# Kernel tuning notes

Hardware: AMD Instinct MI355X
Metric: run time of the kernel (lower is better)

The kernel has to match this reference:

```python
import jax, jax.numpy as jnp
import numpy as np

N, E, IN, HID, OUT = 50000, 800000, 128, 96, 2


def setup_inputs() -> dict:
    key = jax.random.key(0)
    ks = jax.random.split(key, 10)
    x = jax.random.normal(ks[0], (N, IN), jnp.float32)
    edge_index = jax.random.randint(ks[1], (2, E), 0, N, dtype=jnp.int64)
    # PQVA mask: per-node, first output channel is a "known" quantity (masked out),
    # second is the prediction target -> ~mask selects exactly N elements.
    m = np.zeros((N, OUT), dtype=bool)
    m[:, 0] = True
    PQVA_mask = jnp.asarray(m)
    scaler_mean = 0.1 * jax.random.normal(ks[2], (IN,), jnp.float32)
    scaler_std = 0.5 + jax.random.uniform(ks[3], (IN,), jnp.float32)  # in [0.5, 1.5)
    W1 = jax.random.normal(ks[4], (IN, HID), jnp.float32) / np.sqrt(IN)
    W2 = jax.random.normal(ks[5], (HID, HID), jnp.float32) / np.sqrt(HID)
    W3 = jax.random.normal(ks[6], (HID, HID), jnp.float32) / np.sqrt(HID)
    Wout = jax.random.normal(ks[7], (HID, OUT), jnp.float32) / np.sqrt(HID)
    b1 = jnp.zeros((HID,), jnp.float32)
    b2 = jnp.zeros((HID,), jnp.float32)
    b3 = jnp.zeros((HID,), jnp.float32)
    bout = jnp.zeros((OUT,), jnp.float32)
    return {"x": x, "edge_index": edge_index, "PQVA_mask": PQVA_mask,
            "scaler_mean": scaler_mean, "scaler_std": scaler_std,
            "W1": W1, "b1": b1, "W2": W2, "b2": b2, "W3": W3, "b3": b3,
            "Wout": Wout, "bout": bout}


def reference(x, edge_index, PQVA_mask, scaler_mean, scaler_std,
              W1, b1, W2, b2, W3, b3, Wout, bout):
    n = x.shape[0]
    loop = jnp.arange(n, dtype=edge_index.dtype)
    src = jnp.concatenate([edge_index[0], loop])  # add self-loops (GCNConv default)
    dst = jnp.concatenate([edge_index[1], loop])
    deg = jax.ops.segment_sum(jnp.ones_like(dst, x.dtype), dst, num_segments=n)
    dinv = jax.lax.rsqrt(deg)  # deg >= 1 thanks to self-loops
    norm = (dinv[src] * dinv[dst])[:, None]  # [E+N, 1]

    def prop(h):  # D^-1/2 (A+I) D^-1/2 @ h  via gather-scale-scatter
        return jax.ops.segment_sum(h[src] * norm, dst, num_segments=n)

    h = (x - scaler_mean) / scaler_std          # standard scaler
    h = jax.nn.relu(prop(h @ W1) + b1)          # GCNConv 1 + ReLU
    h = jax.nn.relu(prop(h @ W2) + b2)          # GCNConv 2 + ReLU
    h = prop(h @ W3) + b3                       # GCNConv 3 (last, no act)
    out = h @ Wout + bout                       # final Linear -> [N, OUT]
    # masked reshape: ~mask has exactly one True per node -> [N]
    return out.reshape(-1)[~PQVA_mask.reshape(-1)]
```

## Files before the change

kernel.cpp:

```cpp
#include <hip/hip_runtime.h>
#include <hip/hip_fp16.h>

#define IN_F 128
#define HID_F 96
#define PB 512
#define STRIDE 6144
#define MAXB 8192

typedef _Float16 f16x8 __attribute__((ext_vector_type(8)));
typedef float f32x4 __attribute__((ext_vector_type(4)));

__device__ __forceinline__ void swizzle_one(const float* W, __half* Wsw, int idx) {
    int j  = idx & 7;
    int ln = (idx >> 3) & 63;
    int ct = idx >> 9;
    int t = ct % 6, c = ct / 6;
    int k   = c * 32 + (ln >> 4) * 8 + j;
    int col = t * 16 + (ln & 15);
    Wsw[idx] = (__half)W[k * 96 + col];
}

__global__ __launch_bounds__(256) void part_prep_kernel(
        const int* __restrict__ srcv, const int* __restrict__ dstv,
        int* __restrict__ bcur, int* __restrict__ ebuf, int E,
        const float* __restrict__ stdv, float* __restrict__ rstd,
        const float* __restrict__ W3, const float* __restrict__ Wout,
        const float* __restrict__ b3, const float* __restrict__ bout,
        float* __restrict__ wv, float* __restrict__ cconst,
        const float* __restrict__ W1, __half* __restrict__ Wsw1, int SW1,
        const float* __restrict__ W2, __half* __restrict__ Wsw2, int SW2) {
    int b = blockIdx.x, t = threadIdx.x;
    if (b >= PB) {
        int pb = b - PB;
        if (pb == 0) {
            if (t < IN_F) rstd[t] = 1.0f / stdv[t];
            if (t < HID_F) {
                float s = 0.f;
                for (int j = 0; j < HID_F; ++j) s += W3[t * HID_F + j] * Wout[j * 2 + 1];
                wv[t] = s;
            }
            if (t == 0) {
                float s = 0.f;
                for (int j = 0; j < HID_F; ++j) s += b3[j] * Wout[j * 2 + 1];
                cconst[0] = s + bout[1];
            }
        } else if (pb <= 48) {
            int idx = (pb - 1) * 256 + t;
            if (idx < SW1) swizzle_one(W1, Wsw1, idx);
        } else {
            int idx = (pb - 49) * 256 + t;
            if (idx < SW2) swizzle_one(W2, Wsw2, idx);
        }
        return;
    }
    __shared__ int h[256];
    __shared__ int cur[256];
    int chunk = (E + PB - 1) / PB;
    int s = b * chunk;
    int eend = min(s + chunk, E);
    h[t] = 0;
    __syncthreads();
    for (int e = s + t; e < eend; e += 256) atomicAdd(&h[dstv[e] >> 8], 1);
    __syncthreads();
    if (h[t]) cur[t] = t * STRIDE + atomicAdd(&bcur[t], h[t]);
    __syncthreads();
    for (int e = s + t; e < eend; e += 256) {
        int sv = srcv[e], d = dstv[e];
        int p = atomicAdd(&cur[d >> 8], 1);
        ebuf[p] = (sv << 8) | (d & 255);
    }
}


template<int MODE, int K, int SC>
__device__ __forceinline__ void gemm_body(
        int bid, int tid,
        const void* __restrict__ Ain, const __half* __restrict__ Wsw,
        const float* __restrict__ mean, const float* __restrict__ rstd,
        const float* __restrict__ dinv, __half* __restrict__ C, int n) {
    constexpr int NCH = K / 32;
    int lane = tid & 63;
    int wv_  = tid >> 6;
    int m = lane & 15, q = lane >> 4;
    int node0 = bid * 64 + wv_ * 16;
    int g = node0 + m;
    int gc = g < n ? g : n - 1;

    f32x4 acc[6];
#pragma unroll
    for (int t = 0; t < 6; ++t) acc[t] = (f32x4){0.f, 0.f, 0.f, 0.f};

#pragma unroll
    for (int c = 0; c < NCH; ++c) {
        f16x8 a;
        if (MODE == 0) {
            const float* ap = (const float*)Ain + (long)gc * K + c * 32 + q * 8;
            float4 v0 = *(const float4*)ap;
            float4 v1 = *(const float4*)(ap + 4);
            float4 m0 = *(const float4*)(mean + c * 32 + q * 8);
            float4 m1 = *(const float4*)(mean + c * 32 + q * 8 + 4);
            float4 r0 = *(const float4*)(rstd + c * 32 + q * 8);
            float4 r1 = *(const float4*)(rstd + c * 32 + q * 8 + 4);
            a[0] = (_Float16)((v0.x - m0.x) * r0.x);
            a[1] = (_Float16)((v0.y - m0.y) * r0.y);
            a[2] = (_Float16)((v0.z - m0.z) * r0.z);
            a[3] = (_Float16)((v0.w - m0.w) * r0.w);
            a[4] = (_Float16)((v1.x - m1.x) * r1.x);
            a[5] = (_Float16)((v1.y - m1.y) * r1.y);
            a[6] = (_Float16)((v1.z - m1.z) * r1.z);
            a[7] = (_Float16)((v1.w - m1.w) * r1.w);
        } else {
            a = *(const f16x8*)((const __half*)Ain + (long)gc * K + c * 32 + q * 8);
        }
#pragma unroll
        for (int t = 0; t < 6; ++t) {
            f16x8 b = *(const f16x8*)(Wsw + (size_t)(((c * 6) + t) * 64 + lane) * 8);
            acc[t] = __builtin_amdgcn_mfma_f32_16x16x32_f16(a, b, acc[t], 0, 0, 0);
        }
    }
    float dv[4];
#pragma unroll
    for (int r = 0; r < 4; ++r) {
        int gr = node0 + q * 4 + r;
        dv[r] = SC ? ((gr < n) ? dinv[gr] : 0.f) : 1.f;
    }
#pragma unroll
    for (int t = 0; t < 6; ++t)
#pragma unroll
        for (int r = 0; r < 4; ++r) {
            int gr = node0 + q * 4 + r;
            float o = SC ? acc[t][r] * dv[r] : acc[t][r];
            if (gr < n) C[(long)gr * 96 + t * 16 + m] = (__half)o;
        }
}

template<int MODE, int K, int SC>
__global__ __launch_bounds__(256) void gemm_mfma_kernel(
        const void* __restrict__ Ain, const __half* __restrict__ Wsw,
        const float* __restrict__ mean, const float* __restrict__ rstd,
        const float* __restrict__ dinv, __half* __restrict__ C, int n) {
    gemm_body<MODE, K, SC>(blockIdx.x, threadIdx.x, Ain, Wsw, mean, rstd, dinv, C, n);
}


__global__ __launch_bounds__(256) void csr_gemm1_kernel(
        const int* __restrict__ ebuf, const int* __restrict__ bcur,
        int* __restrict__ rowdeg, float* __restrict__ dinv,
        int* __restrict__ cols, int n, int nb,
        const float* __restrict__ x, const __half* __restrict__ Wsw1,
        const float* __restrict__ mean, const float* __restrict__ rstd,
        __half* __restrict__ C) {
    __shared__ int dg[256];
    __shared__ int tmp[256];
    __shared__ int cur[256];
    __shared__ int colst[MAXB];
    int t = threadIdx.x;
    if (blockIdx.x >= nb) {
        gemm_body<0, IN_F, 0>(blockIdx.x - nb, t, x, Wsw1, mean, rstd, nullptr, C, n);
        return;
    }
    int k = blockIdx.x;
    int seg = k * STRIDE;
    int cnt = min(bcur[k], STRIDE);
    dg[t] = 0;
    __syncthreads();
    for (int i = t; i < cnt; i += 256) atomicAdd(&dg[ebuf[seg + i] & 255], 1);
    __syncthreads();
    int v = dg[t];
    tmp[t] = v;
    __syncthreads();
#pragma unroll
    for (int off = 1; off < 256; off <<= 1) {
        int u = (t >= off) ? tmp[t - off] : 0;
        __syncthreads();
        tmp[t] += u;
        __syncthreads();
    }
    int excl = tmp[t] - v;
    int node = (k << 8) + t;
    if (node < n) {
        rowdeg[node] = ((seg + excl) << 9) | v;
        dinv[node] = rsqrtf((float)v + 1.0f);
    }
    cur[t] = excl;
    __syncthreads();
    for (int i = t; i < cnt; i += 256) {
        int p = ebuf[seg + i];
        int lp = atomicAdd(&cur[p & 255], 1);
        colst[lp] = ((unsigned)p) >> 8;
    }
    __syncthreads();
    for (int i = t; i < cnt; i += 256) cols[seg + i] = colst[i];
}


template<int DOT, int SCALE>
__global__ __launch_bounds__(256) void prop4_kernel(
        const __half* __restrict__ hin, const int* __restrict__ rowdeg,
        const int* __restrict__ cols,
        const float* __restrict__ dinv, const float* __restrict__ bias,
        const float* __restrict__ wvv, __half* __restrict__ hout,
        float* __restrict__ zs, int n) {
    int wid  = (blockIdx.x * blockDim.x + threadIdx.x) >> 6;
    int lane = threadIdx.x & 63;
    int g = lane >> 4;
    int l = lane & 15;
    int node = wid * 4 + g;
    bool nvalid = node < n;
    int nodec = nvalid ? node : n - 1;
    int rd = rowdeg[nodec];
    int e0 = ((unsigned)rd) >> 9;
    int deg = rd & 511;
    float di = dinv[nodec];
    const f16x8* hp = (const f16x8*)hin;
    int lc = l < 12 ? l : 0;

    f16x8 vself = hp[(long)nodec * 12 + lc];
    float sself = SCALE ? di : 1.f;
    float acc[8];
#pragma unroll
    for (int j = 0; j < 8; ++j) acc[j] = sself * (float)vself[j];

    for (int eb = 0; eb < deg; eb += 16) {
        int rem = deg - eb;
        if (rem > 16) rem = 16;
        int idx = eb + l;
        int colv = __builtin_nontemporal_load(&cols[e0 + (idx < deg ? idx : 0)]);
        float dvl = SCALE ? dinv[colv] : 1.f;
        for (int k0 = 0; k0 < rem; k0 += 8) {
            int c[8];
            float s[8];
#pragma unroll
            for (int kk = 0; kk < 8; ++kk) {
                int p = k0 + kk;
                int srcl = (g << 4) + p;
                int cc = __shfl(colv, srcl, 64);
                float dd = __shfl(dvl, srcl, 64);
                bool is = p < rem;
                c[kk] = is ? cc : nodec;
                s[kk] = is ? (SCALE ? dd : 1.f) : 0.f;
            }
            f16x8 v[8];
#pragma unroll
            for (int kk = 0; kk < 8; ++kk) v[kk] = hp[(long)c[kk] * 12 + lc];
#pragma unroll
            for (int kk = 0; kk < 8; ++kk)
#pragma unroll
                for (int j = 0; j < 8; ++j)
                    acc[j] = fmaf((float)v[kk][j], s[kk], acc[j]);
        }
    }

    if (DOT == 0) {
        if (nvalid && l < 12) {
            float4 b0 = *(const float4*)(bias + l * 8);
            float4 b1 = *(const float4*)(bias + l * 8 + 4);
            f16x8 o;
            o[0] = (_Float16)fmaxf(di * acc[0] + b0.x, 0.f);
            o[1] = (_Float16)fmaxf(di * acc[1] + b0.y, 0.f);
            o[2] = (_Float16)fmaxf(di * acc[2] + b0.z, 0.f);
            o[3] = (_Float16)fmaxf(di * acc[3] + b0.w, 0.f);
            o[4] = (_Float16)fmaxf(di * acc[4] + b1.x, 0.f);
            o[5] = (_Float16)fmaxf(di * acc[5] + b1.y, 0.f);
            o[6] = (_Float16)fmaxf(di * acc[6] + b1.z, 0.f);
            o[7] = (_Float16)fmaxf(di * acc[7] + b1.w, 0.f);
            __builtin_nontemporal_store(o, (f16x8*)(hout + (long)node * 96 + l * 8));
        }
    } else {
        float v = 0.f;
        if (l < 12) {
            float4 b0 = *(const float4*)(bias + l * 8);
            float4 b1 = *(const float4*)(bias + l * 8 + 4);
            float4 w0 = *(const float4*)(wvv + l * 8);
            float4 w1 = *(const float4*)(wvv + l * 8 + 4);
            v  = fmaxf(di * acc[0] + b0.x, 0.f) * w0.x;
            v += fmaxf(di * acc[1] + b0.y, 0.f) * w0.y;
            v += fmaxf(di * acc[2] + b0.z, 0.f) * w0.z;
            v += fmaxf(di * acc[3] + b0.w, 0.f) * w0.w;
            v += fmaxf(di * acc[4] + b1.x, 0.f) * w1.x;
            v += fmaxf(di * acc[5] + b1.y, 0.f) * w1.y;
            v += fmaxf(di * acc[6] + b1.z, 0.f) * w1.z;
            v += fmaxf(di * acc[7] + b1.w, 0.f) * w1.w;
        }
        v += __shfl_xor(v, 1, 64);
        v += __shfl_xor(v, 2, 64);
        v += __shfl_xor(v, 4, 64);
        v += __shfl_xor(v, 8, 64);
        if (nvalid && l == 0) __builtin_nontemporal_store(di * v, &zs[node]);
    }
}


__global__ __launch_bounds__(256) void prop_scalar_kernel(
        const float* __restrict__ zs, const int* __restrict__ rowdeg,
        const int* __restrict__ cols,
        const float* __restrict__ dinv, const float* __restrict__ cconst,
        float* __restrict__ out, int n) {
    int i = blockIdx.x * blockDim.x + threadIdx.x;
    if (i >= n) return;
    int rd = rowdeg[i];
    int e0 = ((unsigned)rd) >> 9;
    int e1 = e0 + (rd & 511);
    float s = 0.f;
    int e = e0;
    for (; e + 8 <= e1; e += 8) {
        int c[8];
#pragma unroll
        for (int k = 0; k < 8; ++k) c[k] = __builtin_nontemporal_load(&cols[e + k]);
        float z[8];
#pragma unroll
        for (int k = 0; k < 8; ++k) z[k] = zs[c[k]];
#pragma unroll
        for (int k = 0; k < 8; ++k) s += z[k];
    }
    for (; e < e1; ++e) s += zs[__builtin_nontemporal_load(&cols[e])];
    out[i] = dinv[i] * (s + zs[i]) + cconst[0];
}


extern "C" void kernel_launch(void* const* d_in, const int* in_sizes, int n_in,
                              void* d_out, int out_size, void* d_ws, size_t ws_size,
                              hipStream_t stream) {
    const float* x    = (const float*)d_in[0];
    const int*   eidx = (const int*)d_in[1];
    const float* mean = (const float*)d_in[3];
    const float* stdv = (const float*)d_in[4];
    const float* W1   = (const float*)d_in[5];
    const float* b1   = (const float*)d_in[6];
    const float* W2   = (const float*)d_in[7];
    const float* b2   = (const float*)d_in[8];
    const float* W3   = (const float*)d_in[9];
    const float* b3   = (const float*)d_in[10];
    const float* Wout = (const float*)d_in[11];
    const float* bout = (const float*)d_in[12];
    float* out = (float*)d_out;

    const int n = in_sizes[0] / IN_F;
    const int E = in_sizes[1] / 2;
    const int* srcv = eidx;
    const int* dstv = eidx + E;
    const int NB = (n + 255) >> 8;

    char* ws = (char*)d_ws;
    size_t off = 0;
    auto alloc = [&](size_t bytes) -> void* {
        void* p = ws + off;
        off = (off + bytes + 255) & ~(size_t)255;
        return p;
    };
    const int SW1 = 4 * 6 * 64 * 8;
    const int SW2 = 3 * 6 * 64 * 8;
    int*    rowdeg = (int*)alloc((size_t)n * 4);
    float*  dinv   = (float*)alloc((size_t)n * 4);
    int*    cols   = (int*)alloc((size_t)256 * STRIDE * 4);
    int*    ebuf   = (int*)alloc((size_t)256 * STRIDE * 4);
    int*    bcur   = (int*)alloc(256 * 4);
    float*  rstd   = (float*)alloc(IN_F * 4);
    float*  wv     = (float*)alloc(HID_F * 4);
    float*  cconst = (float*)alloc(4);
    float*  zbuf   = (float*)alloc((size_t)n * 4);
    __half* Wsw1   = (__half*)alloc((size_t)SW1 * 2);
    __half* Wsw2   = (__half*)alloc((size_t)SW2 * 2);
    __half* bufA   = (__half*)alloc((size_t)n * HID_F * 2);
    __half* bufB   = (__half*)alloc((size_t)n * HID_F * 2);

    hipMemsetAsync(bcur, 0, 256 * 4, stream);

    part_prep_kernel<<<PB + 85, 256, 0, stream>>>(
        srcv, dstv, bcur, ebuf, E,
        stdv, rstd, W3, Wout, b3, bout, wv, cconst,
        W1, Wsw1, SW1, W2, Wsw2, SW2);

    int gemm_grid = (n + 63) / 64;
    int wpg = (n + 3) / 4;
    int prop_grid = (int)(((long)wpg * 64 + 255) / 256);

    csr_gemm1_kernel<<<NB + gemm_grid, 256, 0, stream>>>(
        ebuf, bcur, rowdeg, dinv, cols, n, NB, x, Wsw1, mean, rstd, bufA);

    prop4_kernel<0, 1><<<prop_grid, 256, 0, stream>>>(bufA, rowdeg, cols, dinv, b1,
                                                      nullptr, bufB, nullptr, n);
    gemm_mfma_kernel<1, HID_F, 1><<<gemm_grid, 256, 0, stream>>>(
        bufB, Wsw2, nullptr, nullptr, dinv, bufA, n);
    prop4_kernel<1, 0><<<prop_grid, 256, 0, stream>>>(bufA, rowdeg, cols, dinv, b2,
                                                      wv, nullptr, zbuf, n);
    prop_scalar_kernel<<<(n + 255) / 256, 256, 0, stream>>>(zbuf, rowdeg, cols, dinv,
                                                            cconst, out, n);
}
```

Baseline: 195.3 us.

## Fuse all GCN stages into one cooperative persistent kernel with grid syncs

Replaces the chain of six kernel launches with a single cooperative persistent kernel whose blocks grid-stride over each stage (partition, CSR build plus first GEMM, two propagations, second GEMM, scalar propagation), separated by grid.sync(). The goal is to remove launch gaps and tail idle time between dependent stages. The cost is grid-wide barriers and a grid capped at 2048 blocks with occupancy hint 4, which may reduce latency hiding in the gather-heavy propagation phases. The shared colst array shrinks from 8192 to STRIDE entries. If the cooperative launch fails, the original separate kernels run instead.

```diff
diff --git a/kernel.cpp b/kernel.cpp
--- a/kernel.cpp
+++ b/kernel.cpp
@@ -1,11 +1,16 @@
 #include <hip/hip_runtime.h>
 #include <hip/hip_fp16.h>
+#include <hip/hip_cooperative_groups.h>
+
+namespace cg = cooperative_groups;
 
 #define IN_F 128
 #define HID_F 96
 #define PB 512
 #define STRIDE 6144
-#define MAXB 8192
+#define SW1C (4 * 6 * 64 * 8)
+#define SW2C (3 * 6 * 64 * 8)
+#define ONE_PASS (1 << 22)
 
 typedef _Float16 f16x8 __attribute__((ext_vector_type(8)));
 typedef float f32x4 __attribute__((ext_vector_type(4)));
@@ -20,57 +25,100 @@
     Wsw[idx] = (__half)W[k * 96 + col];
 }
 
-__global__ __launch_bounds__(256) void part_prep_kernel(
+__device__ __forceinline__ void p0_body(int b0, int bstep, int t,
         const int* __restrict__ srcv, const int* __restrict__ dstv,
         int* __restrict__ bcur, int* __restrict__ ebuf, int E,
         const float* __restrict__ stdv, float* __restrict__ rstd,
         const float* __restrict__ W3, const float* __restrict__ Wout,
         const float* __restrict__ b3, const float* __restrict__ bout,
         float* __restrict__ wv, float* __restrict__ cconst,
-        const float* __restrict__ W1, __half* __restrict__ Wsw1, int SW1,
-        const float* __restrict__ W2, __half* __restrict__ Wsw2, int SW2) {
-    int b = blockIdx.x, t = threadIdx.x;
-    if (b >= PB) {
-        int pb = b - PB;
-        if (pb == 0) {
-            if (t < IN_F) rstd[t] = 1.0f / stdv[t];
-            if (t < HID_F) {
-                float s = 0.f;
-                for (int j = 0; j < HID_F; ++j) s += W3[t * HID_F + j] * Wout[j * 2 + 1];
-                wv[t] = s;
-            }
-            if (t == 0) {
-                float s = 0.f;
-                for (int j = 0; j < HID_F; ++j) s += b3[j] * Wout[j * 2 + 1];
-                cconst[0] = s + bout[1];
-            }
-        } else if (pb <= 48) {
-            int idx = (pb - 1) * 256 + t;
-            if (idx < SW1) swizzle_one(W1, Wsw1, idx);
-        } else {
-            int idx = (pb - 49) * 256 + t;
-            if (idx < SW2) swizzle_one(W2, Wsw2, idx);
-        }
-        return;
-    }
+        const float* __restrict__ W1, __half* __restrict__ Wsw1,
+        const float* __restrict__ W2, __half* __restrict__ Wsw2) {
     __shared__ int h[256];
     __shared__ int cur[256];
-    int chunk = (E + PB - 1) / PB;
-    int s = b * chunk;
-    int eend = min(s + chunk, E);
-    h[t] = 0;
-    __syncthreads();
-    for (int e = s + t; e < eend; e += 256) atomicAdd(&h[dstv[e] >> 8], 1);
-    __syncthreads();
-    if (h[t]) cur[t] = t * STRIDE + atomicAdd(&bcur[t], h[t]);
-    __syncthreads();
-    for (int e = s + t; e < eend; e += 256) {
-        int sv = srcv[e], d = dstv[e];
-        int p = atomicAdd(&cur[d >> 8], 1);
-        ebuf[p] = (sv << 8) | (d & 255);
-    }
-}
-
+    for (int b = b0; b < PB + 85; b += bstep) {
+        if (b >= PB) {
+            int pb = b - PB;
+            if (pb == 0) {
+                if (t < IN_F) rstd[t] = 1.0f / stdv[t];
+                if (t < HID_F) {
+                    float s = 0.f;
+                    for (int j = 0; j < HID_F; ++j) s += W3[t * HID_F + j] * Wout[j * 2 + 1];
+                    wv[t] = s;
+                }
+                if (t == 0) {
+                    float s = 0.f;
+                    for (int j = 0; j < HID_F; ++j) s += b3[j] * Wout[j * 2 + 1];
+                    cconst[0] = s + bout[1];
+                }
+            } else if (pb <= 48) {
+                int idx = (pb - 1) * 256 + t;
+                if (idx < SW1C) swizzle_one(W1, Wsw1, idx);
+            } else {
+                int idx = (pb - 49) * 256 + t;
+                if (idx < SW2C) swizzle_one(W2, Wsw2, idx);
+            }
+            continue;
+        }
+        int chunk = (E + PB - 1) / PB;
+        int s = b * chunk;
+        int eend = min(s + chunk, E);
+        h[t] = 0;
+        __syncthreads();
+        for (int e = s + t; e < eend; e += 256) atomicAdd(&h[dstv[e] >> 8], 1);
+        __syncthreads();
+        if (h[t]) cur[t] = t * STRIDE + atomicAdd(&bcur[t], h[t]);
+        __syncthreads();
+        for (int e = s + t; e < eend; e += 256) {
+            int sv = srcv[e], d = dstv[e];
+            int p = atomicAdd(&cur[d >> 8], 1);
+            ebuf[p] = (sv << 8) | (d & 255);
+        }
+        __syncthreads();
+    }
+}
+
+__device__ __forceinline__ void csr_body(int k, int t,
+        const int* __restrict__ ebuf, const int* __restrict__ bcur,
+        int* __restrict__ rowdeg, float* __restrict__ dinv,
+        int* __restrict__ cols, int n) {
+    __shared__ int dg[256];
+    __shared__ int tmp[256];
+    __shared__ int cur[256];
+    __shared__ int colst[STRIDE];
+    int seg = k * STRIDE;
+    int cnt = min(bcur[k], STRIDE);
+    dg[t] = 0;
+    __syncthreads();
+    for (int i = t; i < cnt; i += 256) atomicAdd(&dg[ebuf[seg + i] & 255], 1);
+    __syncthreads();
+    int v = dg[t];
+    tmp[t] = v;
+    __syncthreads();
+#pragma unroll
+    for (int off = 1; off < 256; off <<= 1) {
+        int u = (t >= off) ? tmp[t - off] : 0;
+        __syncthreads();
+        tmp[t] += u;
+        __syncthreads();
+    }
+    int excl = tmp[t] - v;
+    int node = (k << 8) + t;
+    if (node < n) {
+        rowdeg[node] = ((seg + excl) << 9) | v;
+        dinv[node] = rsqrtf((float)v + 1.0f);
+    }
+    cur[t] = excl;
+    __syncthreads();
+    for (int i = t; i < cnt; i += 256) {
+        int p = ebuf[seg + i];
+        int lp = atomicAdd(&cur[p & 255], 1);
+        colst[lp] = ((unsigned)p) >> 8;
+    }
+    __syncthreads();
+    for (int i = t; i < cnt; i += 256) cols[seg + i] = colst[i];
+    __syncthreads();
+}
 
 template<int MODE, int K, int SC>
 __device__ __forceinline__ void gemm_body(
@@ -134,189 +182,198 @@
         }
 }
 
-template<int MODE, int K, int SC>
-__global__ __launch_bounds__(256) void gemm_mfma_kernel(
-        const void* __restrict__ Ain, const __half* __restrict__ Wsw,
-        const float* __restrict__ mean, const float* __restrict__ rstd,
-        const float* __restrict__ dinv, __half* __restrict__ C, int n) {
-    gemm_body<MODE, K, SC>(blockIdx.x, threadIdx.x, Ain, Wsw, mean, rstd, dinv, C, n);
-}
-
-
-__global__ __launch_bounds__(256) void csr_gemm1_kernel(
-        const int* __restrict__ ebuf, const int* __restrict__ bcur,
-        int* __restrict__ rowdeg, float* __restrict__ dinv,
-        int* __restrict__ cols, int n, int nb,
-        const float* __restrict__ x, const __half* __restrict__ Wsw1,
-        const float* __restrict__ mean, const float* __restrict__ rstd,
-        __half* __restrict__ C) {
-    __shared__ int dg[256];
-    __shared__ int tmp[256];
-    __shared__ int cur[256];
-    __shared__ int colst[MAXB];
-    int t = threadIdx.x;
-    if (blockIdx.x >= nb) {
-        gemm_body<0, IN_F, 0>(blockIdx.x - nb, t, x, Wsw1, mean, rstd, nullptr, C, n);
-        return;
-    }
-    int k = blockIdx.x;
-    int seg = k * STRIDE;
-    int cnt = min(bcur[k], STRIDE);
-    dg[t] = 0;
-    __syncthreads();
-    for (int i = t; i < cnt; i += 256) atomicAdd(&dg[ebuf[seg + i] & 255], 1);
-    __syncthreads();
-    int v = dg[t];
-    tmp[t] = v;
-    __syncthreads();
-#pragma unroll
-    for (int off = 1; off < 256; off <<= 1) {
-        int u = (t >= off) ? tmp[t - off] : 0;
-        __syncthreads();
-        tmp[t] += u;
-        __syncthreads();
-    }
-    int excl = tmp[t] - v;
-    int node = (k << 8) + t;
-    if (node < n) {
-        rowdeg[node] = ((seg + excl) << 9) | v;
-        dinv[node] = rsqrtf((float)v + 1.0f);
-    }
-    cur[t] = excl;
-    __syncthreads();
-    for (int i = t; i < cnt; i += 256) {
-        int p = ebuf[seg + i];
-        int lp = atomicAdd(&cur[p & 255], 1);
-        colst[lp] = ((unsigned)p) >> 8;
-    }
-    __syncthreads();
-    for (int i = t; i < cnt; i += 256) cols[seg + i] = colst[i];
-}
-
-
 template<int DOT, int SCALE>
-__global__ __launch_bounds__(256) void prop4_kernel(
+__device__ __forceinline__ void prop_body(int b0, int bstep, int t,
         const __half* __restrict__ hin, const int* __restrict__ rowdeg,
         const int* __restrict__ cols,
         const float* __restrict__ dinv, const float* __restrict__ bias,
         const float* __restrict__ wvv, __half* __restrict__ hout,
         float* __restrict__ zs, int n) {
-    int wid  = (blockIdx.x * blockDim.x + threadIdx.x) >> 6;
-    int lane = threadIdx.x & 63;
+    int wv_  = t >> 6;
+    int lane = t & 63;
     int g = lane >> 4;
     int l = lane & 15;
-    int node = wid * 4 + g;
-    bool nvalid = node < n;
-    int nodec = nvalid ? node : n - 1;
-    int rd = rowdeg[nodec];
-    int e0 = ((unsigned)rd) >> 9;
-    int deg = rd & 511;
-    float di = dinv[nodec];
+    int lc = l < 12 ? l : 0;
     const f16x8* hp = (const f16x8*)hin;
-    int lc = l < 12 ? l : 0;
-
-    f16x8 vself = hp[(long)nodec * 12 + lc];
-    float sself = SCALE ? di : 1.f;
-    float acc[8];
-#pragma unroll
-    for (int j = 0; j < 8; ++j) acc[j] = sself * (float)vself[j];
-
-    for (int eb = 0; eb < deg; eb += 16) {
-        int rem = deg - eb;
-        if (rem > 16) rem = 16;
-        int idx = eb + l;
-        int colv = __builtin_nontemporal_load(&cols[e0 + (idx < deg ? idx : 0)]);
-        float dvl = SCALE ? dinv[colv] : 1.f;
-        for (int k0 = 0; k0 < rem; k0 += 8) {
-            int c[8];
-            float s[8];
-#pragma unroll
-            for (int kk = 0; kk < 8; ++kk) {
-                int p = k0 + kk;
-                int srcl = (g << 4) + p;
-                int cc = __shfl(colv, srcl, 64);
-                float dd = __shfl(dvl, srcl, 64);
-                bool is = p < rem;
-                c[kk] = is ? cc : nodec;
-                s[kk] = is ? (SCALE ? dd : 1.f) : 0.f;
+    int nblk = (n + 15) >> 4;
+    for (int bb = b0; bb < nblk; bb += bstep) {
+        int node = bb * 16 + wv_ * 4 + g;
+        bool nvalid = node < n;
+        int nodec = nvalid ? node : n - 1;
+        int rd = rowdeg[nodec];
+        int e0 = ((unsigned)rd) >> 9;
+        int deg = rd & 511;
+        float di = dinv[nodec];
+
+        f16x8 vself = hp[(long)nodec * 12 + lc];
+        float sself = SCALE ? di : 1.f;
+        float acc[8];
+#pragma unroll
+        for (int j = 0; j < 8; ++j) acc[j] = sself * (float)vself[j];
+
+        for (int eb = 0; eb < deg; eb += 16) {
+            int rem = deg - eb;
+            if (rem > 16) rem = 16;
+            int idx = eb + l;
+            int colv = __builtin_nontemporal_load(&cols[e0 + (idx < deg ? idx : 0)]);
+            float dvl = SCALE ? dinv[colv] : 1.f;
+            for (int k0 = 0; k0 < rem; k0 += 8) {
+                int c[8];
+                float s[8];
+#pragma unroll
+                for (int kk = 0; kk < 8; ++kk) {
+                    int p = k0 + kk;
+                    int srcl = (g << 4) + p;
+                    int cc = __shfl(colv, srcl, 64);
+                    float dd = __shfl(dvl, srcl, 64);
+                    bool is = p < rem;
+                    c[kk] = is ? cc : nodec;
+                    s[kk] = is ? (SCALE ? dd : 1.f) : 0.f;
+                }
+                f16x8 v[8];
+#pragma unroll
+                for (int kk = 0; kk < 8; ++kk) v[kk] = hp[(long)c[kk] * 12 + lc];
+#pragma unroll
+                for (int kk = 0; kk < 8; ++kk)
+#pragma unroll
+                    for (int j = 0; j < 8; ++j)
+                        acc[j] = fmaf((float)v[kk][j], s[kk], acc[j]);
             }
-            f16x8 v[8];
-#pragma unroll
-            for (int kk = 0; kk < 8; ++kk) v[kk] = hp[(long)c[kk] * 12 + lc];
-#pragma unroll
-            for (int kk = 0; kk < 8; ++kk)
-#pragma unroll
-                for (int j = 0; j < 8; ++j)
-                    acc[j] = fmaf((float)v[kk][j], s[kk], acc[j]);
-        }
-    }
-
-    if (DOT == 0) {
-        if (nvalid && l < 12) {
-            float4 b0 = *(const float4*)(bias + l * 8);
-            float4 b1 = *(const float4*)(bias + l * 8 + 4);
-            f16x8 o;
-            o[0] = (_Float16)fmaxf(di * acc[0] + b0.x, 0.f);
-            o[1] = (_Float16)fmaxf(di * acc[1] + b0.y, 0.f);
-            o[2] = (_Float16)fmaxf(di * acc[2] + b0.z, 0.f);
-            o[3] = (_Float16)fmaxf(di * acc[3] + b0.w, 0.f);
-            o[4] = (_Float16)fmaxf(di * acc[4] + b1.x, 0.f);
-            o[5] = (_Float16)fmaxf(di * acc[5] + b1.y, 0.f);
-            o[6] = (_Float16)fmaxf(di * acc[6] + b1.z, 0.f);
-            o[7] = (_Float16)fmaxf(di * acc[7] + b1.w, 0.f);
-            __builtin_nontemporal_store(o, (f16x8*)(hout + (long)node * 96 + l * 8));
-        }
-    } else {
-        float v = 0.f;
-        if (l < 12) {
-            float4 b0 = *(const float4*)(bias + l * 8);
-            float4 b1 = *(const float4*)(bias + l * 8 + 4);
-            float4 w0 = *(const float4*)(wvv + l * 8);
-            float4 w1 = *(const float4*)(wvv + l * 8 + 4);
-            v  = fmaxf(di * acc[0] + b0.x, 0.f) * w0.x;
-            v += fmaxf(di * acc[1] + b0.y, 0.f) * w0.y;
-            v += fmaxf(di * acc[2] + b0.z, 0.f) * w0.z;
-            v += fmaxf(di * acc[3] + b0.w, 0.f) * w0.w;
-            v += fmaxf(di * acc[4] + b1.x, 0.f) * w1.x;
-            v += fmaxf(di * acc[5] + b1.y, 0.f) * w1.y;
-            v += fmaxf(di * acc[6] + b1.z, 0.f) * w1.z;
-            v += fmaxf(di * acc[7] + b1.w, 0.f) * w1.w;
-        }
-        v += __shfl_xor(v, 1, 64);
-        v += __shfl_xor(v, 2, 64);
-        v += __shfl_xor(v, 4, 64);
-        v += __shfl_xor(v, 8, 64);
-        if (nvalid && l == 0) __builtin_nontemporal_store(di * v, &zs[node]);
-    }
-}
-
-
-__global__ __launch_bounds__(256) void prop_scalar_kernel(
+        }
+
+        if (DOT == 0) {
+            if (nvalid && l < 12) {
+                float4 b0v = *(const float4*)(bias + l * 8);
+                float4 b1v = *(const float4*)(bias + l * 8 + 4);
+                f16x8 o;
+                o[0] = (_Float16)fmaxf(di * acc[0] + b0v.x, 0.f);
+                o[1] = (_Float16)fmaxf(di * acc[1] + b0v.y, 0.f);
+                o[2] = (_Float16)fmaxf(di * acc[2] + b0v.z, 0.f);
+                o[3] = (_Float16)fmaxf(di * acc[3] + b0v.w, 0.f);
+                o[4] = (_Float16)fmaxf(di * acc[4] + b1v.x, 0.f);
+                o[5] = (_Float16)fmaxf(di * acc[5] + b1v.y, 0.f);
+                o[6] = (_Float16)fmaxf(di * acc[6] + b1v.z, 0.f);
+                o[7] = (_Float16)fmaxf(di * acc[7] + b1v.w, 0.f);
+                __builtin_nontemporal_store(o, (f16x8*)(hout + (long)node * 96 + l * 8));
+            }
+        } else {
+            float v = 0.f;
+            if (l < 12) {
+                float4 b0v = *(const float4*)(bias + l * 8);
+                float4 b1v = *(const float4*)(bias + l * 8 + 4);
+                float4 w0 = *(const float4*)(wvv + l * 8);
+                float4 w1 = *(const float4*)(wvv + l * 8 + 4);
+                v  = fmaxf(di * acc[0] + b0v.x, 0.f) * w0.x;
+                v += fmaxf(di * acc[1] + b0v.y, 0.f) * w0.y;
+                v += fmaxf(di * acc[2] + b0v.z, 0.f) * w0.z;
+                v += fmaxf(di * acc[3] + b0v.w, 0.f) * w0.w;
+                v += fmaxf(di * acc[4] + b1v.x, 0.f) * w1.x;
+                v += fmaxf(di * acc[5] + b1v.y, 0.f) * w1.y;
+                v += fmaxf(di * acc[6] + b1v.z, 0.f) * w1.z;
+                v += fmaxf(di * acc[7] + b1v.w, 0.f) * w1.w;
+            }
+            v += __shfl_xor(v, 1, 64);
+            v += __shfl_xor(v, 2, 64);
+            v += __shfl_xor(v, 4, 64);
+            v += __shfl_xor(v, 8, 64);
+            if (nvalid && l == 0) __builtin_nontemporal_store(di * v, &zs[node]);
+        }
+    }
+}
+
+__device__ __forceinline__ void scalar_body(int b0, int bstep, int t,
         const float* __restrict__ zs, const int* __restrict__ rowdeg,
         const int* __restrict__ cols,
         const float* __restrict__ dinv, const float* __restrict__ cconst,
         float* __restrict__ out, int n) {
-    int i = blockIdx.x * blockDim.x + threadIdx.x;
-    if (i >= n) return;
-    int rd = rowdeg[i];
-    int e0 = ((unsigned)rd) >> 9;
-    int e1 = e0 + (rd & 511);
-    float s = 0.f;
-    int e = e0;
-    for (; e + 8 <= e1; e += 8) {
-        int c[8];
-#pragma unroll
-        for (int k = 0; k < 8; ++k) c[k] = __builtin_nontemporal_load(&cols[e + k]);
-        float z[8];
-#pragma unroll
-        for (int k = 0; k < 8; ++k) z[k] = zs[c[k]];
-#pragma unroll
-        for (int k = 0; k < 8; ++k) s += z[k];
-    }
-    for (; e < e1; ++e) s += zs[__builtin_nontemporal_load(&cols[e])];
-    out[i] = dinv[i] * (s + zs[i]) + cconst[0];
-}
-
+    for (int i = b0 * 256 + t; i < n; i += bstep * 256) {
+        int rd = rowdeg[i];
+        int e0 = ((unsigned)rd) >> 9;
+        int e1 = e0 + (rd & 511);
+        float s = 0.f;
+        int e = e0;
+        for (; e + 8 <= e1; e += 8) {
+            int c[8];
+#pragma unroll
+            for (int k = 0; k < 8; ++k) c[k] = __builtin_nontemporal_load(&cols[e + k]);
+            float z[8];
+#pragma unroll
+            for (int k = 0; k < 8; ++k) z[k] = zs[c[k]];
+#pragma unroll
+            for (int k = 0; k < 8; ++k) s += z[k];
+        }
+        for (; e < e1; ++e) s += zs[__builtin_nontemporal_load(&cols[e])];
+        out[i] = dinv[i] * (s + zs[i]) + cconst[0];
+    }
+}
+
+__global__ __launch_bounds__(256, 4) void gcn_mega(
+        const float* x, const int* srcv, const int* dstv, int E, int n,
+        const float* mean, const float* stdv,
+        const float* W1, const float* b1, const float* W2, const float* b2,
+        const float* W3, const float* b3, const float* Wout, const float* bout,
+        int* bcur, int* ebuf, int* rowdeg, float* dinv, int* cols,
+        float* rstd, float* wvv, float* cconst, float* zbuf,
+        __half* Wsw1, __half* Wsw2, __half* bufA, __half* bufB, float* out) {
+    cg::grid_group grid = cg::this_grid();
+    int b = blockIdx.x, t = threadIdx.x, G = gridDim.x;
+    int nbuck = (n + 255) >> 8;
+    int gg = (n + 63) >> 6;
+
+    p0_body(b, G, t, srcv, dstv, bcur, ebuf, E, stdv, rstd,
+            W3, Wout, b3, bout, wvv, cconst, W1, Wsw1, W2, Wsw2);
+    grid.sync();
+    for (int bb = b; bb < nbuck + gg; bb += G) {
+        if (bb < nbuck) csr_body(bb, t, ebuf, bcur, rowdeg, dinv, cols, n);
+        else gemm_body<0, IN_F, 0>(bb - nbuck, t, x, Wsw1, mean, rstd, nullptr, bufA, n);
+    }
+    grid.sync();
+    prop_body<0, 1>(b, G, t, bufA, rowdeg, cols, dinv, b1, nullptr, bufB, nullptr, n);
+    grid.sync();
+    for (int bb = b; bb < gg; bb += G)
+        gemm_body<1, HID_F, 1>(bb, t, bufB, Wsw2, nullptr, nullptr, dinv, bufA, n);
+    grid.sync();
+    prop_body<1, 0>(b, G, t, bufA, rowdeg, cols, dinv, b2, wvv, nullptr, zbuf, n);
+    grid.sync();
+    scalar_body(b, G, t, zbuf, rowdeg, cols, dinv, cconst, out, n);
+}
+
+__global__ __launch_bounds__(256) void fb_p0(
+        const int* srcv, const int* dstv, int* bcur, int* ebuf, int E,
+        const float* stdv, float* rstd, const float* W3, const float* Wout,
+        const float* b3, const float* bout, float* wvv, float* cconst,
+        const float* W1, __half* Wsw1, const float* W2, __half* Wsw2) {
+    p0_body(blockIdx.x, ONE_PASS, threadIdx.x, srcv, dstv, bcur, ebuf, E,
+            stdv, rstd, W3, Wout, b3, bout, wvv, cconst, W1, Wsw1, W2, Wsw2);
+}
+
+__global__ __launch_bounds__(256) void fb_csr_gemm1(
+        const int* ebuf, const int* bcur, int* rowdeg, float* dinv, int* cols,
+        int n, int nb, const float* x, const __half* Wsw1,
+        const float* mean, const float* rstd, __half* C) {
+    int b = blockIdx.x, t = threadIdx.x;
+    if (b < nb) csr_body(b, t, ebuf, bcur, rowdeg, dinv, cols, n);
+    else gemm_body<0, IN_F, 0>(b - nb, t, x, Wsw1, mean, rstd, nullptr, C, n);
+}
+
+template<int DOT, int SCALE>
+__global__ __launch_bounds__(256) void fb_prop(
+        const __half* hin, const int* rowdeg, const int* cols, const float* dinv,
+        const float* bias, const float* wvv, __half* hout, float* zs, int n) {
+    prop_body<DOT, SCALE>(blockIdx.x, ONE_PASS, threadIdx.x,
+                          hin, rowdeg, cols, dinv, bias, wvv, hout, zs, n);
+}
+
+__global__ __launch_bounds__(256) void fb_gemm2(
+        const __half* A, const __half* Wsw, const float* dinv, __half* C, int n) {
+    gemm_body<1, HID_F, 1>(blockIdx.x, threadIdx.x, A, Wsw, nullptr, nullptr, dinv, C, n);
+}
+
+__global__ __launch_bounds__(256) void fb_scalar(
+        const float* zs, const int* rowdeg, const int* cols, const float* dinv,
+        const float* cconst, float* out, int n) {
+    scalar_body(blockIdx.x, ONE_PASS, threadIdx.x, zs, rowdeg, cols, dinv, cconst, out, n);
+}
 
 extern "C" void kernel_launch(void* const* d_in, const int* in_sizes, int n_in,
                               void* d_out, int out_size, void* d_ws, size_t ws_size,
@@ -335,8 +392,8 @@
     const float* bout = (const float*)d_in[12];
     float* out = (float*)d_out;
 
-    const int n = in_sizes[0] / IN_F;
-    const int E = in_sizes[1] / 2;
+    int n = in_sizes[0] / IN_F;
+    int E = in_sizes[1] / 2;
     const int* srcv = eidx;
     const int* dstv = eidx + E;
     const int NB = (n + 255) >> 8;
@@ -348,42 +405,59 @@
         off = (off + bytes + 255) & ~(size_t)255;
         return p;
     };
-    const int SW1 = 4 * 6 * 64 * 8;
-    const int SW2 = 3 * 6 * 64 * 8;
     int*    rowdeg = (int*)alloc((size_t)n * 4);
     float*  dinv   = (float*)alloc((size_t)n * 4);
     int*    cols   = (int*)alloc((size_t)256 * STRIDE * 4);
     int*    ebuf   = (int*)alloc((size_t)256 * STRIDE * 4);
     int*    bcur   = (int*)alloc(256 * 4);
     float*  rstd   = (float*)alloc(IN_F * 4);
-    float*  wv     = (float*)alloc(HID_F * 4);
+    float*  wvv    = (float*)alloc(HID_F * 4);
     float*  cconst = (float*)alloc(4);
     float*  zbuf   = (float*)alloc((size_t)n * 4);
-    __half* Wsw1   = (__half*)alloc((size_t)SW1 * 2);
-    __half* Wsw2   = (__half*)alloc((size_t)SW2 * 2);
+    __half* Wsw1   = (__half*)alloc((size_t)SW1C * 2);
+    __half* Wsw2   = (__half*)alloc((size_t)SW2C * 2);
     __half* bufA   = (__half*)alloc((size_t)n * HID_F * 2);
     __half* bufB   = (__half*)alloc((size_t)n * HID_F * 2);
 
     hipMemsetAsync(bcur, 0, 256 * 4, stream);
 
-    part_prep_kernel<<<PB + 85, 256, 0, stream>>>(
-        srcv, dstv, bcur, ebuf, E,
-        stdv, rstd, W3, Wout, b3, bout, wv, cconst,
-        W1, Wsw1, SW1, W2, Wsw2, SW2);
-
-    int gemm_grid = (n + 63) / 64;
-    int wpg = (n + 3) / 4;
-    int prop_grid = (int)(((long)wpg * 64 + 255) / 256);
-
-    csr_gemm1_kernel<<<NB + gemm_grid, 256, 0, stream>>>(
-        ebuf, bcur, rowdeg, dinv, cols, n, NB, x, Wsw1, mean, rstd, bufA);
-
-    prop4_kernel<0, 1><<<prop_grid, 256, 0, stream>>>(bufA, rowdeg, cols, dinv, b1,
-                                                      nullptr, bufB, nullptr, n);
-    gemm_mfma_kernel<1, HID_F, 1><<<gemm_grid, 256, 0, stream>>>(
-        bufB, Wsw2, nullptr, nullptr, dinv, bufA, n);
-    prop4_kernel<1, 0><<<prop_grid, 256, 0, stream>>>(bufA, rowdeg, cols, dinv, b2,
-                                                      wv, nullptr, zbuf, n);
-    prop_scalar_kernel<<<(n + 255) / 256, 256, 0, stream>>>(zbuf, rowdeg, cols, dinv,
-                                                            cconst, out, n);
-}
+    static int coopG = -2;
+    if (coopG == -2) {
+        int mb = 0;
+        if (hipOccupancyMaxActiveBlocksPerMultiprocessor(&mb, gcn_mega, 256, 0)
+                != hipSuccess) mb = 0;
+        coopG = (mb >= 1) ? mb * 256 : 0;
+        if (coopG > 2048) coopG = 2048;
+    }
+
+    bool done = false;
+    if (coopG >= 256) {
+        void* kargs[] = {
+            (void*)&x, (void*)&srcv, (void*)&dstv, (void*)&E, (void*)&n,
+            (void*)&mean, (void*)&stdv,
+            (void*)&W1, (void*)&b1, (void*)&W2, (void*)&b2,
+            (void*)&W3, (void*)&b3, (void*)&Wout, (void*)&bout,
+            (void*)&bcur, (void*)&ebuf, (void*)&rowdeg, (void*)&dinv, (void*)&cols,
+            (void*)&rstd, (void*)&wvv, (void*)&cconst, (void*)&zbuf,
+            (void*)&Wsw1, (void*)&Wsw2, (void*)&bufA, (void*)&bufB, (void*)&out };
+        done = hipLaunchCooperativeKernel(gcn_mega, dim3(coopG), dim3(256),
+                                          kargs, 0, stream) == hipSuccess;
+    }
+
+    if (!done) {
+        int gemm_grid = (n + 63) / 64;
+        int prop_grid = (n + 15) / 16;
+        fb_p0<<<PB + 85, 256, 0, stream>>>(srcv, dstv, bcur, ebuf, E, stdv, rstd,
+                                           W3, Wout, b3, bout, wvv, cconst,
+                                           W1, Wsw1, W2, Wsw2);
+        fb_csr_gemm1<<<NB + gemm_grid, 256, 0, stream>>>(ebuf, bcur, rowdeg, dinv, cols,
+                                                         n, NB, x, Wsw1, mean, rstd, bufA);
+        fb_prop<0, 1><<<prop_grid, 256, 0, stream>>>(bufA, rowdeg, cols, dinv, b1,
+                                                     nullptr, bufB, nullptr, n);
+        fb_gemm2<<<gemm_grid, 256, 0, stream>>>(bufB, Wsw2, dinv, bufA, n);
+        fb_prop<1, 0><<<prop_grid, 256, 0, stream>>>(bufA, rowdeg, cols, dinv, b2,
+                                                     wvv, nullptr, zbuf, n);
+        fb_scalar<<<(n + 255) / 256, 256, 0, stream>>>(zbuf, rowdeg, cols, dinv,
+                                                       cconst, out, n);
+    }
+}
```

Measured after the change: 544.3 us. 2.79x slower.

## Fuse first propagation with second-layer MFMA GEMM via shared memory tile

Applied to the files above, without the earlier changes.

Replaces the separate prop4 (layer 1 aggregation + bias + ReLU) and gemm_mfma (layer 2 matmul scaled by dinv) launches with one kernel. Each block aggregates 64 nodes' neighbor features into an LDS tile, then runs the MFMA GEMM on that tile directly. This removes one launch and the fp16 intermediate write and reread of the [N,96] hidden buffer. The price is a block-wide barrier between the irregular gather phase and the GEMM, which can let slow high-degree nodes hold up the whole block, plus the LDS use affects occupancy.

```diff
diff --git a/kernel.cpp b/kernel.cpp
--- a/kernel.cpp
+++ b/kernel.cpp
@@ -71,7 +71,6 @@
     }
 }
 
-
 template<int MODE, int K, int SC>
 __device__ __forceinline__ void gemm_body(
         int bid, int tid,
@@ -134,15 +133,6 @@
         }
 }
 
-template<int MODE, int K, int SC>
-__global__ __launch_bounds__(256) void gemm_mfma_kernel(
-        const void* __restrict__ Ain, const __half* __restrict__ Wsw,
-        const float* __restrict__ mean, const float* __restrict__ rstd,
-        const float* __restrict__ dinv, __half* __restrict__ C, int n) {
-    gemm_body<MODE, K, SC>(blockIdx.x, threadIdx.x, Ain, Wsw, mean, rstd, dinv, C, n);
-}
-
-
 __global__ __launch_bounds__(256) void csr_gemm1_kernel(
         const int* __restrict__ ebuf, const int* __restrict__ bcur,
         int* __restrict__ rowdeg, float* __restrict__ dinv,
@@ -193,6 +183,111 @@
     for (int i = t; i < cnt; i += 256) cols[seg + i] = colst[i];
 }
 
+
+__global__ __launch_bounds__(256) void prop1_gemm2_kernel(
+        const __half* __restrict__ hin, const int* __restrict__ rowdeg,
+        const int* __restrict__ cols, const float* __restrict__ dinv,
+        const float* __restrict__ bias, const __half* __restrict__ Wsw2,
+        __half* __restrict__ Cout, int n) {
+    __shared__ __half hs[64][104];
+    int t = threadIdx.x;
+    int wv_  = t >> 6;
+    int lane = t & 63;
+    int g = lane >> 4;
+    int l = lane & 15;
+    int lc = l < 12 ? l : 0;
+    const f16x8* hp = (const f16x8*)hin;
+    int base = blockIdx.x * 64;
+
+    for (int it = 0; it < 4; ++it) {
+        int local = wv_ * 16 + it * 4 + g;
+        int node = base + local;
+        bool nvalid = node < n;
+        int nodec = nvalid ? node : n - 1;
+        int rd = rowdeg[nodec];
+        int e0 = ((unsigned)rd) >> 9;
+        int deg = rd & 511;
+        float di = dinv[nodec];
+
+        f16x8 vself = hp[(long)nodec * 12 + lc];
+        float acc[8];
+#pragma unroll
+        for (int j = 0; j < 8; ++j) acc[j] = di * (float)vself[j];
+
+        for (int eb = 0; eb < deg; eb += 16) {
+            int rem = deg - eb;
+            if (rem > 16) rem = 16;
+            int idx = eb + l;
+            int colv = __builtin_nontemporal_load(&cols[e0 + (idx < deg ? idx : 0)]);
+            float dvl = dinv[colv];
+            for (int k0 = 0; k0 < rem; k0 += 8) {
+                int c[8];
+                float s[8];
+#pragma unroll
+                for (int kk = 0; kk < 8; ++kk) {
+                    int p = k0 + kk;
+                    int srcl = (g << 4) + p;
+                    int cc = __shfl(colv, srcl, 64);
+                    float dd = __shfl(dvl, srcl, 64);
+                    bool is = p < rem;
+                    c[kk] = is ? cc : nodec;
+                    s[kk] = is ? dd : 0.f;
+                }
+                f16x8 v[8];
+#pragma unroll
+                for (int kk = 0; kk < 8; ++kk) v[kk] = hp[(long)c[kk] * 12 + lc];
+#pragma unroll
+                for (int kk = 0; kk < 8; ++kk)
+#pragma unroll
+                    for (int j = 0; j < 8; ++j)
+                        acc[j] = fmaf((float)v[kk][j], s[kk], acc[j]);
+            }
+        }
+        if (l < 12) {
+            float4 b0 = *(const float4*)(bias + l * 8);
+            float4 b1v = *(const float4*)(bias + l * 8 + 4);
+            f16x8 o;
+            o[0] = (_Float16)fmaxf(di * acc[0] + b0.x, 0.f);
+            o[1] = (_Float16)fmaxf(di * acc[1] + b0.y, 0.f);
+            o[2] = (_Float16)fmaxf(di * acc[2] + b0.z, 0.f);
+            o[3] = (_Float16)fmaxf(di * acc[3] + b0.w, 0.f);
+            o[4] = (_Float16)fmaxf(di * acc[4] + b1v.x, 0.f);
+            o[5] = (_Float16)fmaxf(di * acc[5] + b1v.y, 0.f);
+            o[6] = (_Float16)fmaxf(di * acc[6] + b1v.z, 0.f);
+            o[7] = (_Float16)fmaxf(di * acc[7] + b1v.w, 0.f);
+            *(f16x8*)&hs[local][l * 8] = o;
+        }
+    }
+    __syncthreads();
+
+    int m = lane & 15, q = lane >> 4;
+    int node0 = base + wv_ * 16;
+    f32x4 acc2[6];
+#pragma unroll
+    for (int tt = 0; tt < 6; ++tt) acc2[tt] = (f32x4){0.f, 0.f, 0.f, 0.f};
+#pragma unroll
+    for (int c = 0; c < 3; ++c) {
+        f16x8 a = *(const f16x8*)&hs[wv_ * 16 + m][c * 32 + q * 8];
+#pragma unroll
+        for (int tt = 0; tt < 6; ++tt) {
+            f16x8 b = *(const f16x8*)(Wsw2 + (size_t)(((c * 6) + tt) * 64 + lane) * 8);
+            acc2[tt] = __builtin_amdgcn_mfma_f32_16x16x32_f16(a, b, acc2[tt], 0, 0, 0);
+        }
+    }
+    float dv[4];
+#pragma unroll
+    for (int r = 0; r < 4; ++r) {
+        int gr = node0 + q * 4 + r;
+        dv[r] = (gr < n) ? dinv[gr] : 0.f;
+    }
+#pragma unroll
+    for (int tt = 0; tt < 6; ++tt)
+#pragma unroll
+        for (int r = 0; r < 4; ++r) {
+            int gr = node0 + q * 4 + r;
+            if (gr < n) Cout[(long)gr * 96 + tt * 16 + m] = (__half)(acc2[tt][r] * dv[r]);
+        }
+}
 
 template<int DOT, int SCALE>
 __global__ __launch_bounds__(256) void prop4_kernel(
@@ -290,7 +385,6 @@
     }
 }
 
-
 __global__ __launch_bounds__(256) void prop_scalar_kernel(
         const float* __restrict__ zs, const int* __restrict__ rowdeg,
         const int* __restrict__ cols,
@@ -316,7 +410,6 @@
     for (; e < e1; ++e) s += zs[__builtin_nontemporal_load(&cols[e])];
     out[i] = dinv[i] * (s + zs[i]) + cconst[0];
 }
-
 
 extern "C" void kernel_launch(void* const* d_in, const int* in_sizes, int n_in,
                               void* d_out, int out_size, void* d_ws, size_t ws_size,
@@ -356,7 +449,7 @@
     int*    ebuf   = (int*)alloc((size_t)256 * STRIDE * 4);
     int*    bcur   = (int*)alloc(256 * 4);
     float*  rstd   = (float*)alloc(IN_F * 4);
-    float*  wv     = (float*)alloc(HID_F * 4);
+    float*  wvv    = (float*)alloc(HID_F * 4);
     float*  cconst = (float*)alloc(4);
     float*  zbuf   = (float*)alloc((size_t)n * 4);
     __half* Wsw1   = (__half*)alloc((size_t)SW1 * 2);
@@ -368,22 +461,20 @@
 
     part_prep_kernel<<<PB + 85, 256, 0, stream>>>(
         srcv, dstv, bcur, ebuf, E,
-        stdv, rstd, W3, Wout, b3, bout, wv, cconst,
+        stdv, rstd, W3, Wout, b3, bout, wvv, cconst,
         W1, Wsw1, SW1, W2, Wsw2, SW2);
 
     int gemm_grid = (n + 63) / 64;
-    int wpg = (n + 3) / 4;
-    int prop_grid = (int)(((long)wpg * 64 + 255) / 256);
+    int prop_grid = (n + 15) / 16;
 
     csr_gemm1_kernel<<<NB + gemm_grid, 256, 0, stream>>>(
         ebuf, bcur, rowdeg, dinv, cols, n, NB, x, Wsw1, mean, rstd, bufA);
 
-    prop4_kernel<0, 1><<<prop_grid, 256, 0, stream>>>(bufA, rowdeg, cols, dinv, b1,
-                                                      nullptr, bufB, nullptr, n);
-    gemm_mfma_kernel<1, HID_F, 1><<<gemm_grid, 256, 0, stream>>>(
-        bufB, Wsw2, nullptr, nullptr, dinv, bufA, n);
-    prop4_kernel<1, 0><<<prop_grid, 256, 0, stream>>>(bufA, rowdeg, cols, dinv, b2,
-                                                      wv, nullptr, zbuf, n);
+    prop1_gemm2_kernel<<<gemm_grid, 256, 0, stream>>>(
+        bufA, rowdeg, cols, dinv, b1, Wsw2, bufB, n);
+
+    prop4_kernel<1, 0><<<prop_grid, 256, 0, stream>>>(bufB, rowdeg, cols, dinv, b2,
+                                                      wvv, nullptr, zbuf, n);
     prop_scalar_kernel<<<(n + 255) / 256, 256, 0, stream>>>(zbuf, rowdeg, cols, dinv,
                                                             cconst, out, n);
 }
```

Result: slower. 203.6 us (+4.3%).
